# Kernel optimization log

Hardware: AMD Instinct MI355X
Metric: run time of the kernel (lower is better)

Reference implementation:

```python
import jax, jax.numpy as jnp
import numpy as np

EPS = 1e-5

def _bn(x, g, b, m, v):
    # inference-mode batchnorm with moving statistics
    return (x - m) * jax.lax.rsqrt(v + EPS) * g + b

def setup_inputs() -> dict:
    key = jax.random.key(0)
    ks = jax.random.split(key, 12)
    t, b, s, hu = 512, 64, 1024, 1024
    d_in = s + hu
    si = jax.random.normal(ks[0], (b, s), dtype=jnp.float32)
    h = jax.random.normal(ks[1], (t, b, hu), dtype=jnp.float32)
    W0 = jax.random.normal(ks[2], (d_in, 10), dtype=jnp.float32) * 0.02
    b0 = jnp.zeros((10,), jnp.float32)
    g0 = jnp.ones((10,), jnp.float32)
    be0 = jnp.zeros((10,), jnp.float32)
    m0 = jax.random.normal(ks[3], (10,), dtype=jnp.float32) * 0.1
    v0 = jax.random.uniform(ks[4], (10,), dtype=jnp.float32) + 0.5
    W1 = jax.random.normal(ks[5], (10, 5), dtype=jnp.float32) * 0.3
    b1 = jnp.zeros((5,), jnp.float32)
    g1 = jnp.ones((5,), jnp.float32)
    be1 = jnp.zeros((5,), jnp.float32)
    m1 = jax.random.normal(ks[6], (5,), dtype=jnp.float32) * 0.1
    v1 = jax.random.uniform(ks[7], (5,), dtype=jnp.float32) + 0.5
    W2 = jax.random.normal(ks[8], (5, 1), dtype=jnp.float32) * 0.4
    b2 = jnp.zeros((1,), jnp.float32)
    return {"si": si, "h": h, "W0": W0, "b0": b0, "g0": g0, "be0": be0,
            "m0": m0, "v0": v0, "W1": W1, "b1": b1, "g1": g1, "be1": be1,
            "m1": m1, "v1": v1, "W2": W2, "b2": b2}

def reference(si, h, W0, b0, g0, be0, m0, v0, W1, b1, g1, be1, m1, v1, W2, b2):
    t, b, hu = h.shape
    # concat decoder state with every encoder hidden state: [t, b, s+hu]
    x = jnp.concatenate([jnp.broadcast_to(si[None], (t,) + si.shape), h], axis=-1)
    x = jax.nn.relu(_bn(x @ W0 + b0, g0, be0, m0, v0))
    x = jax.nn.relu(_bn(x @ W1 + b1, g1, be1, m1, v1))
    scores = x @ W2 + b2                       # [t, b, 1]
    # original: tf.concat over axis 0 -> [t*b, 1], softmax over axis 0 (ALL t*b entries)
    a = jax.nn.softmax(scores.reshape(t * b))  # [t*b]
    # original uses only the first t rows of the flattened softmax as scalar weights
    ci = jnp.einsum('t,tbh->bh', a[:t], h)     # [b, hu]
    return ci
```

## Files before the change

### kernel.cpp

```cpp
#include <hip/hip_runtime.h>

#define EPS 1e-5f

constexpr int T  = 512;
constexpr int B  = 64;
constexpr int HU = 1024;
constexpr int S  = 1024;
constexpr int P  = T * B;
constexpr int C  = B * HU;
constexpr int TSPLIT = 32;

constexpr size_t OFF_W    = 1024;
constexpr size_t OFF_ZB   = 2048;
constexpr size_t OFF_PART = 35840;

__global__ __launch_bounds__(512) void k_scores(
    const float* __restrict__ h,  const float* __restrict__ si,
    const float* __restrict__ W0,
    const float* __restrict__ b0, const float* __restrict__ g0,
    const float* __restrict__ be0,const float* __restrict__ m0,
    const float* __restrict__ v0,
    const float* __restrict__ W1, const float* __restrict__ b1,
    const float* __restrict__ g1, const float* __restrict__ be1,
    const float* __restrict__ m1, const float* __restrict__ v1,
    const float* __restrict__ W2, const float* __restrict__ b2,
    float* __restrict__ wout, float* __restrict__ Zb) {
    const int g   = blockIdx.x;
    const int tid = threadIdx.x;
    const int wv  = tid >> 6;
    const int ln  = tid & 63;
    const int p   = g * 64 + ln;
    const float* hrow = h  + (size_t)p  * HU;
    const float* srow = si + (size_t)ln * S;
    const int k0 = __builtin_amdgcn_readfirstlane(wv * 128);

    float acc[10];
#pragma unroll
    for (int j = 0; j < 10; ++j) acc[j] = 0.f;

#pragma unroll 4
    for (int i = 0; i < 32; ++i) {
        const int k = k0 + 4 * i;
        const float4 hv = *(const float4*)(hrow + k);
        const float4 sv = *(const float4*)(srow + k);
        const float* wph = W0 + (size_t)(1024 + k) * 10;
        const float* wps = W0 + (size_t)k * 10;
#pragma unroll
        for (int d = 0; d < 4; ++d) {
            const float hx = (&hv.x)[d];
            const float sx = (&sv.x)[d];
#pragma unroll
            for (int j = 0; j < 10; ++j)
                acc[j] = fmaf(hx, wph[d * 10 + j], acc[j]);
#pragma unroll
            for (int j = 0; j < 10; ++j)
                acc[j] = fmaf(sx, wps[d * 10 + j], acc[j]);
        }
    }

    __shared__ float part[8][64][10];
#pragma unroll
    for (int j = 0; j < 10; ++j) part[wv][ln][j] = acc[j];
    __syncthreads();

    if (wv == 0) {
        float y[10];
#pragma unroll
        for (int j = 0; j < 10; ++j) {
            float u = b0[j];
#pragma unroll
            for (int w = 0; w < 8; ++w) u += part[w][ln][j];
            u = (u - m0[j]) * (1.0f / sqrtf(v0[j] + EPS)) * g0[j] + be0[j];
            y[j] = fmaxf(u, 0.f);
        }
        float z[5];
#pragma unroll
        for (int i = 0; i < 5; ++i) {
            float u = b1[i];
#pragma unroll
            for (int j = 0; j < 10; ++j) u = fmaf(y[j], W1[j * 5 + i], u);
            u = (u - m1[i]) * (1.0f / sqrtf(v1[i] + EPS)) * g1[i] + be1[i];
            z[i] = fmaxf(u, 0.f);
        }
        float sc = b2[0];
#pragma unroll
        for (int i = 0; i < 5; ++i) sc = fmaf(z[i], W2[i], sc);

        const float e = expf(sc);
        float zsum = e;
#pragma unroll
        for (int off = 32; off > 0; off >>= 1)
            zsum += __shfl_down(zsum, off, 64);
        if (ln == 0) Zb[g] = zsum;
        if (g < 8) wout[p] = e;
    }
}

__global__ __launch_bounds__(256) void k_wsum(const float* __restrict__ h,
                                              const float* __restrict__ w,
                                              float* __restrict__ part) {
    const int cb = blockIdx.x & 63;
    const int ts = blockIdx.x >> 6;
    const int c  = cb * 1024 + threadIdx.x * 4;
    const float* hp = h + (size_t)ts * 16 * C + c;
    const float* ap = w + ts * 16;

    float4 acc = {0.f, 0.f, 0.f, 0.f};
#pragma unroll
    for (int i = 0; i < 16; ++i) {
        const float av = ap[i];
        const float4 hv = *(const float4*)(hp + (size_t)i * C);
        acc.x = fmaf(av, hv.x, acc.x);
        acc.y = fmaf(av, hv.y, acc.y);
        acc.z = fmaf(av, hv.z, acc.z);
        acc.w = fmaf(av, hv.w, acc.w);
    }
    *(float4*)(part + (size_t)ts * C + c) = acc;
}

__global__ __launch_bounds__(64) void k_reduce(const float* __restrict__ part,
                                               const float* __restrict__ Zb,
                                               float* __restrict__ out) {
    const int tid = threadIdx.x;

    const float4 z0 = ((const float4*)Zb)[tid * 2];
    const float4 z1 = ((const float4*)Zb)[tid * 2 + 1];
    float zs = z0.x + z0.y + z0.z + z0.w + z1.x + z1.y + z1.z + z1.w;
#pragma unroll
    for (int off = 32; off > 0; off >>= 1)
        zs += __shfl_down(zs, off, 64);
    const float invZ = 1.0f / __shfl(zs, 0, 64);

    const int c = blockIdx.x * 256 + tid * 4;
    float4 s = {0.f, 0.f, 0.f, 0.f};
#pragma unroll 8
    for (int ts = 0; ts < TSPLIT; ++ts) {
        const float4 v = *(const float4*)(part + (size_t)ts * C + c);
        s.x += v.x; s.y += v.y; s.z += v.z; s.w += v.w;
    }
    s.x *= invZ; s.y *= invZ; s.z *= invZ; s.w *= invZ;
    *(float4*)(out + c) = s;
}

extern "C" void kernel_launch(void* const* d_in, const int* in_sizes, int n_in,
                              void* d_out, int out_size, void* d_ws, size_t ws_size,
                              hipStream_t stream) {
    const float* si  = (const float*)d_in[0];
    const float* h   = (const float*)d_in[1];
    const float* W0  = (const float*)d_in[2];
    const float* b0  = (const float*)d_in[3];
    const float* g0  = (const float*)d_in[4];
    const float* be0 = (const float*)d_in[5];
    const float* m0  = (const float*)d_in[6];
    const float* v0  = (const float*)d_in[7];
    const float* W1  = (const float*)d_in[8];
    const float* b1  = (const float*)d_in[9];
    const float* g1  = (const float*)d_in[10];
    const float* be1 = (const float*)d_in[11];
    const float* m1  = (const float*)d_in[12];
    const float* v1  = (const float*)d_in[13];
    const float* W2  = (const float*)d_in[14];
    const float* b2  = (const float*)d_in[15];

    float* ws   = (float*)d_ws;
    float* w    = ws + OFF_W;
    float* Zb   = ws + OFF_ZB;
    float* part = ws + OFF_PART;
    float* out  = (float*)d_out;

    hipLaunchKernelGGL(k_scores, dim3(512),  dim3(512), 0, stream, h, si, W0,
                       b0, g0, be0, m0, v0, W1, b1, g1, be1, m1, v1, W2, b2, w, Zb);
    hipLaunchKernelGGL(k_wsum,   dim3(2048), dim3(256), 0, stream, h, w, part);
    hipLaunchKernelGGL(k_reduce, dim3(256),  dim3(64),  0, stream, part, Zb, out);
}
```

Baseline: 273.7 us.

## Precompute si·W0 once and stage h tiles through LDS in score kernel

The si part of the first matmul does not depend on t, so it is computed once per batch row in a new small kernel and added as a bias, instead of being recomputed for every t. The h part now loads coalesced 64x128 tiles into padded shared memory, prefetching the next chunk into registers, and each wave reduces over a 16-column slice. This removes half the FMAs and the redundant si reads, and replaces strided per-row loads with coalesced ones. In exchange it adds an extra launch and per-chunk barriers.

```diff
diff --git a/kernel.cpp b/kernel.cpp
--- a/kernel.cpp
+++ b/kernel.cpp
@@ -10,13 +10,49 @@
 constexpr int C  = B * HU;
 constexpr int TSPLIT = 32;
 
+constexpr size_t OFF_SIW0 = 0;
 constexpr size_t OFF_W    = 1024;
 constexpr size_t OFF_ZB   = 2048;
 constexpr size_t OFF_PART = 35840;
 
+__global__ __launch_bounds__(256) void k_siw0(const float* __restrict__ si,
+                                              const float* __restrict__ W0,
+                                              float* __restrict__ out) {
+    const int b   = blockIdx.x;
+    const int tid = threadIdx.x;
+    const float4 sv = ((const float4*)(si + (size_t)b * S))[tid];
+    const float* wp = W0 + (size_t)(4 * tid) * 10;
+
+    float acc[10];
+#pragma unroll
+    for (int j = 0; j < 10; ++j) acc[j] = 0.f;
+#pragma unroll
+    for (int d = 0; d < 4; ++d) {
+        const float hx = (&sv.x)[d];
+#pragma unroll
+        for (int j = 0; j < 10; ++j) acc[j] = fmaf(hx, wp[d * 10 + j], acc[j]);
+    }
+#pragma unroll
+    for (int j = 0; j < 10; ++j) {
+#pragma unroll
+        for (int off = 32; off > 0; off >>= 1)
+            acc[j] += __shfl_down(acc[j], off, 64);
+    }
+    __shared__ float red[4][10];
+    const int wv = tid >> 6, ln = tid & 63;
+    if (ln == 0) {
+#pragma unroll
+        for (int j = 0; j < 10; ++j) red[wv][j] = acc[j];
+    }
+    __syncthreads();
+    if (tid < 10)
+        out[(size_t)b * 10 + tid] =
+            red[0][tid] + red[1][tid] + red[2][tid] + red[3][tid];
+}
+
 __global__ __launch_bounds__(512) void k_scores(
-    const float* __restrict__ h,  const float* __restrict__ si,
-    const float* __restrict__ W0,
+    const float* __restrict__ h,  const float* __restrict__ W0,
+    const float* __restrict__ siW0,
     const float* __restrict__ b0, const float* __restrict__ g0,
     const float* __restrict__ be0,const float* __restrict__ m0,
     const float* __restrict__ v0,
@@ -25,40 +61,67 @@
     const float* __restrict__ m1, const float* __restrict__ v1,
     const float* __restrict__ W2, const float* __restrict__ b2,
     float* __restrict__ wout, float* __restrict__ Zb) {
+    constexpr int KC   = 128;
+    constexpr int NCH  = HU / KC;
+    constexpr int LDR  = KC + 1;
+
+    __shared__ float sh[64 * LDR];
+    __shared__ float part[8][64][10];
+
     const int g   = blockIdx.x;
     const int tid = threadIdx.x;
     const int wv  = tid >> 6;
     const int ln  = tid & 63;
-    const int p   = g * 64 + ln;
-    const float* hrow = h  + (size_t)p  * HU;
-    const float* srow = si + (size_t)ln * S;
-    const int k0 = __builtin_amdgcn_readfirstlane(wv * 128);
+    const float* hbase = h + (size_t)g * 64 * HU;
+
+    int rr[4], cc[4];
+#pragma unroll
+    for (int q = 0; q < 4; ++q) {
+        const int f = tid + 512 * q;
+        rr[q] = f >> 5;
+        cc[q] = (f & 31) * 4;
+    }
+
+    float4 stg[4];
+#pragma unroll
+    for (int q = 0; q < 4; ++q)
+        stg[q] = *(const float4*)(hbase + (size_t)rr[q] * HU + cc[q]);
+
+    const int klo = __builtin_amdgcn_readfirstlane(16 * wv);
 
     float acc[10];
 #pragma unroll
     for (int j = 0; j < 10; ++j) acc[j] = 0.f;
 
-#pragma unroll 4
-    for (int i = 0; i < 32; ++i) {
-        const int k = k0 + 4 * i;
-        const float4 hv = *(const float4*)(hrow + k);
-        const float4 sv = *(const float4*)(srow + k);
-        const float* wph = W0 + (size_t)(1024 + k) * 10;
-        const float* wps = W0 + (size_t)k * 10;
-#pragma unroll
-        for (int d = 0; d < 4; ++d) {
-            const float hx = (&hv.x)[d];
-            const float sx = (&sv.x)[d];
+    for (int c = 0; c < NCH; ++c) {
+        if (c > 0) __syncthreads();
+#pragma unroll
+        for (int q = 0; q < 4; ++q) {
+            float* dst = sh + rr[q] * LDR + cc[q];
+            dst[0] = stg[q].x; dst[1] = stg[q].y;
+            dst[2] = stg[q].z; dst[3] = stg[q].w;
+        }
+        if (c + 1 < NCH) {
+#pragma unroll
+            for (int q = 0; q < 4; ++q)
+                stg[q] = *(const float4*)(hbase + (size_t)rr[q] * HU +
+                                          (c + 1) * KC + cc[q]);
+        }
+        __syncthreads();
+
+        const float* wp0 = W0 + (size_t)(1024 + c * KC + klo) * 10;
+        const float* shp = sh + ln * LDR + klo;
+#pragma unroll
+        for (int kk = 0; kk < 16; ++kk) {
+            const float hv = shp[kk];
+            const float* wp = wp0 + kk * 10;
 #pragma unroll
             for (int j = 0; j < 10; ++j)
-                acc[j] = fmaf(hx, wph[d * 10 + j], acc[j]);
-#pragma unroll
-            for (int j = 0; j < 10; ++j)
-                acc[j] = fmaf(sx, wps[d * 10 + j], acc[j]);
-        }
-    }
-
-    __shared__ float part[8][64][10];
+                acc[j] = fmaf(hv, wp[j], acc[j]);
+        }
+    }
+
+    __syncthreads();
 #pragma unroll
     for (int j = 0; j < 10; ++j) part[wv][ln][j] = acc[j];
     __syncthreads();
@@ -67,7 +130,7 @@
         float y[10];
 #pragma unroll
         for (int j = 0; j < 10; ++j) {
-            float u = b0[j];
+            float u = siW0[(size_t)ln * 10 + j] + b0[j];
 #pragma unroll
             for (int w = 0; w < 8; ++w) u += part[w][ln][j];
             u = (u - m0[j]) * (1.0f / sqrtf(v0[j] + EPS)) * g0[j] + be0[j];
@@ -92,7 +155,7 @@
         for (int off = 32; off > 0; off >>= 1)
             zsum += __shfl_down(zsum, off, 64);
         if (ln == 0) Zb[g] = zsum;
-        if (g < 8) wout[p] = e;
+        if (g < 8) wout[g * 64 + ln] = e;
     }
 }
 
@@ -163,12 +226,14 @@
     const float* b2  = (const float*)d_in[15];
 
     float* ws   = (float*)d_ws;
+    float* siW0 = ws + OFF_SIW0;
     float* w    = ws + OFF_W;
     float* Zb   = ws + OFF_ZB;
     float* part = ws + OFF_PART;
     float* out  = (float*)d_out;
 
-    hipLaunchKernelGGL(k_scores, dim3(512),  dim3(512), 0, stream, h, si, W0,
+    hipLaunchKernelGGL(k_siw0,   dim3(64),   dim3(256), 0, stream, si, W0, siW0);
+    hipLaunchKernelGGL(k_scores, dim3(512),  dim3(512), 0, stream, h, W0, siW0,
                        b0, g0, be0, m0, v0, W1, b1, g1, be1, m1, v1, W2, b2, w, Zb);
     hipLaunchKernelGGL(k_wsum,   dim3(2048), dim3(256), 0, stream, h, w, part);
     hipLaunchKernelGGL(k_reduce, dim3(256),  dim3(64),  0, stream, part, Zb, out);
```

Result: faster. 257.5 us (-5.9%).

## Fuse score computation into weighted-sum pass so h is streamed once

Applied to the files above, without the earlier changes.

The score MLP is split out: a small kernel computes si@W0 once per batch row, plus the exp-weights for the first 8 t-steps needed by the weighted sum. The main kernel then computes the h@W0 projections for all rows and the weighted partial sums in the same streaming pass over h. This removes the separate full read of h that the old score kernel did. In exchange it adds per-iteration wave shuffle reductions, more register pressure from the 40 cached W0 values, and a final kernel that reduces all 32768 exp scores in every block.

```diff
diff --git a/kernel.cpp b/kernel.cpp
--- a/kernel.cpp
+++ b/kernel.cpp
@@ -6,15 +6,46 @@
 constexpr int B  = 64;
 constexpr int HU = 1024;
 constexpr int S  = 1024;
-constexpr int P  = T * B;
 constexpr int C  = B * HU;
 constexpr int TSPLIT = 32;
 
+constexpr size_t OFF_SIW0 = 0;
 constexpr size_t OFF_W    = 1024;
-constexpr size_t OFF_ZB   = 2048;
+constexpr size_t OFF_ESC  = 2048;
 constexpr size_t OFF_PART = 35840;
 
-__global__ __launch_bounds__(512) void k_scores(
+__device__ __forceinline__ float mlp_head(
+    const float* __restrict__ u10,
+    const float* __restrict__ b0, const float* __restrict__ g0,
+    const float* __restrict__ be0,const float* __restrict__ m0,
+    const float* __restrict__ v0,
+    const float* __restrict__ W1, const float* __restrict__ b1,
+    const float* __restrict__ g1, const float* __restrict__ be1,
+    const float* __restrict__ m1, const float* __restrict__ v1,
+    const float* __restrict__ W2, const float* __restrict__ b2) {
+    float y[10];
+#pragma unroll
+    for (int j = 0; j < 10; ++j) {
+        float u = (u10[j] + b0[j] - m0[j]) * (1.0f / sqrtf(v0[j] + EPS)) * g0[j]
+                  + be0[j];
+        y[j] = fmaxf(u, 0.f);
+    }
+    float z[5];
+#pragma unroll
+    for (int i = 0; i < 5; ++i) {
+        float u = b1[i];
+#pragma unroll
+        for (int j = 0; j < 10; ++j) u = fmaf(y[j], W1[j * 5 + i], u);
+        u = (u - m1[i]) * (1.0f / sqrtf(v1[i] + EPS)) * g1[i] + be1[i];
+        z[i] = fmaxf(u, 0.f);
+    }
+    float sc = b2[0];
+#pragma unroll
+    for (int i = 0; i < 5; ++i) sc = fmaf(z[i], W2[i], sc);
+    return sc;
+}
+
+__global__ __launch_bounds__(256) void k_weights(
     const float* __restrict__ h,  const float* __restrict__ si,
     const float* __restrict__ W0,
     const float* __restrict__ b0, const float* __restrict__ g0,
@@ -24,114 +55,168 @@
     const float* __restrict__ g1, const float* __restrict__ be1,
     const float* __restrict__ m1, const float* __restrict__ v1,
     const float* __restrict__ W2, const float* __restrict__ b2,
-    float* __restrict__ wout, float* __restrict__ Zb) {
-    const int g   = blockIdx.x;
+    float* __restrict__ w, float* __restrict__ siW0out) {
+    const int e   = blockIdx.x;
+    const int t   = e >> 6;
+    const int cb  = e & 63;
     const int tid = threadIdx.x;
-    const int wv  = tid >> 6;
-    const int ln  = tid & 63;
-    const int p   = g * 64 + ln;
-    const float* hrow = h  + (size_t)p  * HU;
-    const float* srow = si + (size_t)ln * S;
-    const int k0 = __builtin_amdgcn_readfirstlane(wv * 128);
-
-    float acc[10];
-#pragma unroll
-    for (int j = 0; j < 10; ++j) acc[j] = 0.f;
+    const int wv  = tid >> 6, ln = tid & 63;
+
+    const float4 hv = *(const float4*)(h  + (size_t)t  * C + (size_t)cb * HU + tid * 4);
+    const float4 sv = *(const float4*)(si + (size_t)cb * S + tid * 4);
+    const float* wsb = W0 + (size_t)(4 * tid) * 10;
+    const float* whb = W0 + (size_t)(1024 + 4 * tid) * 10;
+
+    float ssi[10], shh[10];
+#pragma unroll
+    for (int j = 0; j < 10; ++j) { ssi[j] = 0.f; shh[j] = 0.f; }
+#pragma unroll
+    for (int d = 0; d < 4; ++d) {
+        const float sx = (&sv.x)[d], hx = (&hv.x)[d];
+#pragma unroll
+        for (int j = 0; j < 10; ++j) {
+            ssi[j] = fmaf(sx, wsb[d * 10 + j], ssi[j]);
+            shh[j] = fmaf(hx, whb[d * 10 + j], shh[j]);
+        }
+    }
+#pragma unroll
+    for (int j = 0; j < 10; ++j) {
+#pragma unroll
+        for (int off = 32; off > 0; off >>= 1) {
+            ssi[j] += __shfl_down(ssi[j], off, 64);
+            shh[j] += __shfl_down(shh[j], off, 64);
+        }
+    }
+    __shared__ float rs[4][10], rh[4][10];
+    if (ln == 0) {
+#pragma unroll
+        for (int j = 0; j < 10; ++j) { rs[wv][j] = ssi[j]; rh[wv][j] = shh[j]; }
+    }
+    __syncthreads();
+
+    if (t == 0 && tid < 10)
+        siW0out[cb * 10 + tid] = rs[0][tid] + rs[1][tid] + rs[2][tid] + rs[3][tid];
+
+    if (tid == 0) {
+        float u10[10];
+#pragma unroll
+        for (int j = 0; j < 10; ++j)
+            u10[j] = rs[0][j] + rs[1][j] + rs[2][j] + rs[3][j] +
+                     rh[0][j] + rh[1][j] + rh[2][j] + rh[3][j];
+        const float sc = mlp_head(u10, b0, g0, be0, m0, v0,
+                                  W1, b1, g1, be1, m1, v1, W2, b2);
+        w[t * 64 + cb] = expf(sc);
+    }
+}
+
+__global__ __launch_bounds__(256) void k_fused(
+    const float* __restrict__ h,  const float* __restrict__ W0,
+    const float* __restrict__ w,  const float* __restrict__ siW0,
+    const float* __restrict__ b0, const float* __restrict__ g0,
+    const float* __restrict__ be0,const float* __restrict__ m0,
+    const float* __restrict__ v0,
+    const float* __restrict__ W1, const float* __restrict__ b1,
+    const float* __restrict__ g1, const float* __restrict__ be1,
+    const float* __restrict__ m1, const float* __restrict__ v1,
+    const float* __restrict__ W2, const float* __restrict__ b2,
+    float* __restrict__ escore, float* __restrict__ part) {
+    const int cb  = blockIdx.x & 63;
+    const int ts  = blockIdx.x >> 6;
+    const int tid = threadIdx.x;
+    const int wv  = tid >> 6, ln = tid & 63;
+
+    float wf[40];
+    {
+        const float4* wb = (const float4*)(W0 + (size_t)(1024 + 4 * tid) * 10);
+#pragma unroll
+        for (int q = 0; q < 10; ++q) {
+            const float4 v4 = wb[q];
+            wf[4 * q + 0] = v4.x; wf[4 * q + 1] = v4.y;
+            wf[4 * q + 2] = v4.z; wf[4 * q + 3] = v4.w;
+        }
+    }
+
+    __shared__ float red[4][16][10];
+
+    const float* hp = h + (size_t)(ts * 16) * C + (size_t)cb * HU + tid * 4;
+    const float* wt = w + ts * 16;
+
+    float4 wacc = {0.f, 0.f, 0.f, 0.f};
+    float4 hv = *(const float4*)(hp);
 
 #pragma unroll 4
-    for (int i = 0; i < 32; ++i) {
-        const int k = k0 + 4 * i;
-        const float4 hv = *(const float4*)(hrow + k);
-        const float4 sv = *(const float4*)(srow + k);
-        const float* wph = W0 + (size_t)(1024 + k) * 10;
-        const float* wps = W0 + (size_t)k * 10;
+    for (int i = 0; i < 16; ++i) {
+        const float4 hcur = hv;
+        if (i + 1 < 16)
+            hv = *(const float4*)(hp + (size_t)(i + 1) * C);
+
+        const float av = wt[i];
+        wacc.x = fmaf(av, hcur.x, wacc.x);
+        wacc.y = fmaf(av, hcur.y, wacc.y);
+        wacc.z = fmaf(av, hcur.z, wacc.z);
+        wacc.w = fmaf(av, hcur.w, wacc.w);
+
+        float sacc[10];
+#pragma unroll
+        for (int j = 0; j < 10; ++j) sacc[j] = 0.f;
 #pragma unroll
         for (int d = 0; d < 4; ++d) {
-            const float hx = (&hv.x)[d];
-            const float sx = (&sv.x)[d];
+            const float hx = (&hcur.x)[d];
 #pragma unroll
             for (int j = 0; j < 10; ++j)
-                acc[j] = fmaf(hx, wph[d * 10 + j], acc[j]);
-#pragma unroll
-            for (int j = 0; j < 10; ++j)
-                acc[j] = fmaf(sx, wps[d * 10 + j], acc[j]);
-        }
-    }
-
-    __shared__ float part[8][64][10];
-#pragma unroll
-    for (int j = 0; j < 10; ++j) part[wv][ln][j] = acc[j];
-    __syncthreads();
-
-    if (wv == 0) {
-        float y[10];
+                sacc[j] = fmaf(hx, wf[d * 10 + j], sacc[j]);
+        }
 #pragma unroll
         for (int j = 0; j < 10; ++j) {
-            float u = b0[j];
-#pragma unroll
-            for (int w = 0; w < 8; ++w) u += part[w][ln][j];
-            u = (u - m0[j]) * (1.0f / sqrtf(v0[j] + EPS)) * g0[j] + be0[j];
-            y[j] = fmaxf(u, 0.f);
-        }
-        float z[5];
-#pragma unroll
-        for (int i = 0; i < 5; ++i) {
-            float u = b1[i];
-#pragma unroll
-            for (int j = 0; j < 10; ++j) u = fmaf(y[j], W1[j * 5 + i], u);
-            u = (u - m1[i]) * (1.0f / sqrtf(v1[i] + EPS)) * g1[i] + be1[i];
-            z[i] = fmaxf(u, 0.f);
-        }
-        float sc = b2[0];
-#pragma unroll
-        for (int i = 0; i < 5; ++i) sc = fmaf(z[i], W2[i], sc);
-
-        const float e = expf(sc);
-        float zsum = e;
-#pragma unroll
-        for (int off = 32; off > 0; off >>= 1)
-            zsum += __shfl_down(zsum, off, 64);
-        if (ln == 0) Zb[g] = zsum;
-        if (g < 8) wout[p] = e;
-    }
-}
-
-__global__ __launch_bounds__(256) void k_wsum(const float* __restrict__ h,
-                                              const float* __restrict__ w,
-                                              float* __restrict__ part) {
-    const int cb = blockIdx.x & 63;
-    const int ts = blockIdx.x >> 6;
-    const int c  = cb * 1024 + threadIdx.x * 4;
-    const float* hp = h + (size_t)ts * 16 * C + c;
-    const float* ap = w + ts * 16;
-
-    float4 acc = {0.f, 0.f, 0.f, 0.f};
-#pragma unroll
-    for (int i = 0; i < 16; ++i) {
-        const float av = ap[i];
-        const float4 hv = *(const float4*)(hp + (size_t)i * C);
-        acc.x = fmaf(av, hv.x, acc.x);
-        acc.y = fmaf(av, hv.y, acc.y);
-        acc.z = fmaf(av, hv.z, acc.z);
-        acc.w = fmaf(av, hv.w, acc.w);
-    }
-    *(float4*)(part + (size_t)ts * C + c) = acc;
-}
-
-__global__ __launch_bounds__(64) void k_reduce(const float* __restrict__ part,
-                                               const float* __restrict__ Zb,
-                                               float* __restrict__ out) {
+#pragma unroll
+            for (int off = 32; off > 0; off >>= 1)
+                sacc[j] += __shfl_down(sacc[j], off, 64);
+        }
+        if (ln == 0) {
+#pragma unroll
+            for (int j = 0; j < 10; ++j) red[wv][i][j] = sacc[j];
+        }
+    }
+
+    *(float4*)(part + (size_t)ts * C + (size_t)cb * HU + tid * 4) = wacc;
+
+    __syncthreads();
+    if (tid < 16) {
+        float u10[10];
+#pragma unroll
+        for (int j = 0; j < 10; ++j)
+            u10[j] = red[0][tid][j] + red[1][tid][j] + red[2][tid][j] +
+                     red[3][tid][j] + siW0[cb * 10 + j];
+        const float sc = mlp_head(u10, b0, g0, be0, m0, v0,
+                                  W1, b1, g1, be1, m1, v1, W2, b2);
+        escore[(ts * 16 + tid) * 64 + cb] = expf(sc);
+    }
+}
+
+__global__ __launch_bounds__(256) void k_out(const float* __restrict__ part,
+                                             const float* __restrict__ escore,
+                                             float* __restrict__ out) {
     const int tid = threadIdx.x;
-
-    const float4 z0 = ((const float4*)Zb)[tid * 2];
-    const float4 z1 = ((const float4*)Zb)[tid * 2 + 1];
-    float zs = z0.x + z0.y + z0.z + z0.w + z1.x + z1.y + z1.z + z1.w;
+    const int wv  = tid >> 6, ln = tid & 63;
+
+    float zs = 0.f;
+#pragma unroll
+    for (int q = 0; q < 32; ++q) {
+        const float4 v = ((const float4*)escore)[tid + 256 * q];
+        zs += v.x + v.y + v.z + v.w;
+    }
 #pragma unroll
     for (int off = 32; off > 0; off >>= 1)
         zs += __shfl_down(zs, off, 64);
-    const float invZ = 1.0f / __shfl(zs, 0, 64);
-
-    const int c = blockIdx.x * 256 + tid * 4;
+    __shared__ float zr[4];
+    __shared__ float sinv;
+    if (ln == 0) zr[wv] = zs;
+    __syncthreads();
+    if (tid == 0) sinv = 1.0f / (zr[0] + zr[1] + zr[2] + zr[3]);
+    __syncthreads();
+    const float invZ = sinv;
+
+    const int c = blockIdx.x * 1024 + tid * 4;
     float4 s = {0.f, 0.f, 0.f, 0.f};
 #pragma unroll 8
     for (int ts = 0; ts < TSPLIT; ++ts) {
@@ -162,14 +247,18 @@
     const float* W2  = (const float*)d_in[14];
     const float* b2  = (const float*)d_in[15];
 
-    float* ws   = (float*)d_ws;
-    float* w    = ws + OFF_W;
-    float* Zb   = ws + OFF_ZB;
-    float* part = ws + OFF_PART;
-    float* out  = (float*)d_out;
-
-    hipLaunchKernelGGL(k_scores, dim3(512),  dim3(512), 0, stream, h, si, W0,
-                       b0, g0, be0, m0, v0, W1, b1, g1, be1, m1, v1, W2, b2, w, Zb);
-    hipLaunchKernelGGL(k_wsum,   dim3(2048), dim3(256), 0, stream, h, w, part);
-    hipLaunchKernelGGL(k_reduce, dim3(256),  dim3(64),  0, stream, part, Zb, out);
-}
+    float* ws     = (float*)d_ws;
+    float* siW0   = ws + OFF_SIW0;
+    float* w      = ws + OFF_W;
+    float* escore = ws + OFF_ESC;
+    float* part   = ws + OFF_PART;
+    float* out    = (float*)d_out;
+
+    hipLaunchKernelGGL(k_weights, dim3(512),  dim3(256), 0, stream, h, si, W0,
+                       b0, g0, be0, m0, v0, W1, b1, g1, be1, m1, v1, W2, b2,
+                       w, siW0);
+    hipLaunchKernelGGL(k_fused,   dim3(2048), dim3(256), 0, stream, h, W0, w, siW0,
+                       b0, g0, be0, m0, v0, W1, b1, g1, be1, m1, v1, W2, b2,
+                       escore, part);
+    hipLaunchKernelGGL(k_out,     dim3(64),   dim3(256), 0, stream, part, escore, out);
+}
```

New measurement: 283.7 us. 1.04x slower.
